# Performance work log

Measured on AMD Instinct MI355X. Metric: run time of the kernel, lower is better.

## Reference

```python
import jax, jax.numpy as jnp
import numpy as np


def setup_inputs() -> dict:
    key = jax.random.key(0)
    k1, k2 = jax.random.split(key)
    N, D = 8192, 256
    cond_feature = jax.random.normal(k1, (N, D), dtype=jnp.float32)
    sol_feature = jax.random.normal(k2, (N, D), dtype=jnp.float32)
    temperature = jnp.asarray(0.5, dtype=jnp.float32)  # learned scalar, used as exp(temperature)
    return {"cond_feature": cond_feature, "sol_feature": sol_feature, "temperature": temperature}


def reference(cond_feature, sol_feature, temperature):
    N = cond_feature.shape[0]
    c = cond_feature.reshape(N, -1)  # [N, D]
    s = sol_feature.reshape(sol_feature.shape[0], -1)  # [N, D]
    # pairwise L2 distance via ||a||^2 + ||b||^2 - 2 a.b (avoids N x N x D intermediate)
    c2 = jnp.sum(c * c, axis=-1)  # [N]
    s2 = jnp.sum(s * s, axis=-1)  # [N]
    d2 = c2[:, None] + s2[None, :] - 2.0 * jnp.einsum('nd,md->nm', c, s)
    dist = jnp.sqrt(jnp.maximum(d2, 0.0))  # [N, N]
    sim = -dist * jnp.exp(temperature)
    # cross_entropy(sim, arange) + cross_entropy(sim.T, arange): diagonal of log-softmax both ways
    logp_row = jax.nn.log_softmax(sim, axis=-1)  # CE over rows
    logp_col = jax.nn.log_softmax(sim, axis=0)   # CE over columns == CE(sim.T, labels)
    diag = jnp.arange(N)
    loss_row = -jnp.mean(logp_row[diag, diag])
    loss_col = -jnp.mean(logp_col[diag, diag])
    return (loss_row + loss_col) * 0.5
```

## Files before the change

kernel.cpp:

```cpp
#include <hip/hip_runtime.h>
#include <math.h>

#define DIM 256
#define TM 256
#define TN 128

typedef int   v4i   __attribute__((ext_vector_type(4)));
typedef int   v8i   __attribute__((ext_vector_type(8)));
typedef float f32x16 __attribute__((ext_vector_type(16)));

typedef const __attribute__((address_space(1))) void* gas_ptr;
typedef __attribute__((address_space(3))) void* las_ptr;

__device__ __forceinline__ void async_cp16(const void* g, void* l) {
    __builtin_amdgcn_global_load_lds((gas_ptr)g, (las_ptr)l, 16, 0, 0);
}

__global__ __launch_bounds__(256) void convert_kernel(
        const float* __restrict__ C, const float* __restrict__ S,
        unsigned char* __restrict__ Cb, unsigned char* __restrict__ Sb,
        float* __restrict__ c2, float* __restrict__ s2,
        float* __restrict__ ddot, float* __restrict__ sums0,
        float* __restrict__ out, int N) {
    int gtid = blockIdx.x * 256 + threadIdx.x;
    if (gtid < 2 * N) sums0[gtid] = 0.0f;
    if (gtid == 0) out[0] = 0.0f;
    int row = gtid >> 6;
    int l = gtid & 63;
    if (row >= N) return;
    float4 v  = ((const float4*)(C + (size_t)row * DIM))[l];
    float4 sv = ((const float4*)(S + (size_t)row * DIM))[l];
    int pc = __builtin_amdgcn_cvt_pk_fp8_f32(v.x, v.y, 0, false);
    pc     = __builtin_amdgcn_cvt_pk_fp8_f32(v.z, v.w, pc, true);
    int ps = __builtin_amdgcn_cvt_pk_fp8_f32(sv.x, sv.y, 0, false);
    ps     = __builtin_amdgcn_cvt_pk_fp8_f32(sv.z, sv.w, ps, true);
    int idx4 = (row >> 5) * 2048 + (l >> 4) * 512 + ((l >> 2) & 1) * 256
             + ((row & 31) + 32 * ((l >> 3) & 1)) * 4 + (l & 3);
    ((int*)Cb)[idx4] = pc;
    ((int*)Sb)[idx4] = ps;
    float nc = v.x * v.x + v.y * v.y + v.z * v.z + v.w * v.w;
    float ns = sv.x * sv.x + sv.y * sv.y + sv.z * sv.z + sv.w * sv.w;
    float cr = v.x * sv.x + v.y * sv.y + v.z * sv.z + v.w * sv.w;
    #pragma unroll
    for (int off = 32; off > 0; off >>= 1) {
        nc += __shfl_down(nc, off, 64);
        ns += __shfl_down(ns, off, 64);
        cr += __shfl_down(cr, off, 64);
    }
    if (l == 0) { c2[row] = nc; s2[row] = ns; ddot[row] = cr; }
}

__global__ __launch_bounds__(512, 4) void mfma_kernel(
        const unsigned char* __restrict__ Cb, const unsigned char* __restrict__ Sb,
        const float* __restrict__ c2, const float* __restrict__ s2,
        const float* __restrict__ temp,
        float* __restrict__ rowsum, float* __restrict__ colsum, int N) {
    __shared__ __align__(16) unsigned char Abuf[TM * 64];
    __shared__ __align__(16) unsigned char Bbuf[TN * 64];
    __shared__ float rs[TM], cs[TN], c2t[TM], s2t[TN];

    const int tid = threadIdx.x;
    const int bm = blockIdx.y * TM;
    const int bn = blockIdx.x * TN;
    const int w  = tid >> 6;
    const int l  = tid & 63;
    const int wm = (w >> 1) * 64;
    const int wn = (w & 1) * 64;

    const float escale = __expf(temp[0]);
    const float Kf = escale * 1.4426950408889634f;
    const float K2 = Kf * Kf;
    const float m2K2 = -2.0f * K2;

    if (tid < TM) { rs[tid] = 0.0f; c2t[tid] = K2 * c2[bm + tid]; }
    else if (tid < TM + TN) {
        int t = tid - TM; cs[t] = 0.0f; s2t[t] = K2 * s2[bn + t];
    }

    const unsigned char* gA = Cb + (size_t)((bm >> 5) + w) * 8192 + (size_t)l * 16;
    const unsigned char* gB = Sb + (size_t)((bn >> 5) + (w >> 1)) * 8192
                                 + (size_t)(w & 1) * 1024 + (size_t)l * 16;
    unsigned char* lA = &Abuf[w * 2048];
    unsigned char* lB = &Bbuf[(w >> 1) * 2048 + (w & 1) * 1024];

    const int abase = (w >> 1) * 4096 + l * 16;
    const int bbase = (w & 1) * 4096 + l * 16;

    f32x16 acc[2][2] = {};

    #pragma unroll
    for (int kk = 0; kk < 4; ++kk) {
        async_cp16(gA, lA);
        async_cp16(gA + 1024, lA + 1024);
        async_cp16(gB, lB);
        gA += 2048; gB += 2048;
        __syncthreads();

        v8i af[2], bf[2];
        #pragma unroll
        for (int t = 0; t < 2; ++t) {
            v4i alo = *(const v4i*)&Abuf[abase + t * 2048];
            v4i ahi = *(const v4i*)&Abuf[abase + t * 2048 + 1024];
            af[t] = __builtin_shufflevector(alo, ahi, 0, 1, 2, 3, 4, 5, 6, 7);
            v4i blo = *(const v4i*)&Bbuf[bbase + t * 2048];
            v4i bhi = *(const v4i*)&Bbuf[bbase + t * 2048 + 1024];
            bf[t] = __builtin_shufflevector(blo, bhi, 0, 1, 2, 3, 4, 5, 6, 7);
        }
        #pragma unroll
        for (int mi = 0; mi < 2; ++mi)
            #pragma unroll
            for (int ni = 0; ni < 2; ++ni)
                acc[mi][ni] = __builtin_amdgcn_mfma_scale_f32_32x32x64_f8f6f4(
                    af[mi], bf[ni], acc[mi][ni], 0, 0,
                    0, 0x7F, 0, 0x7F);
        __syncthreads();
    }

    const int q2 = l >> 5;
    const int col5 = l & 31;
    float s2v[2] = { s2t[wn + col5], s2t[wn + 32 + col5] };

    float rfold[2];
    float cp[2] = {0.f, 0.f};

    #pragma unroll
    for (int mi = 0; mi < 2; ++mi) {
        float c2r[16];
        #pragma unroll
        for (int s = 0; s < 16; ++s)
            c2r[s] = c2t[wm + mi * 32 + (s & 3) + 8 * (s >> 2) + 4 * q2];
        float rp[16];
        #pragma unroll
        for (int s = 0; s < 16; ++s) rp[s] = 0.0f;
        #pragma unroll
        for (int ni = 0; ni < 2; ++ni) {
            #pragma unroll
            for (int s = 0; s < 16; ++s) {
                float d2 = fmaf(m2K2, acc[mi][ni][s], c2r[s] + s2v[ni]);
                d2 = fmaxf(d2, 0.0f);
                float e = __builtin_amdgcn_exp2f(-__builtin_amdgcn_sqrtf(d2));
                rp[s] += e;
                cp[ni] += e;
            }
        }
        #pragma unroll
        for (int b = 0; b < 4; ++b) {
            const int n = 16 >> b;
            const int bit = (l >> b) & 1;
            #pragma unroll
            for (int k = 0; k < 8; ++k) {
                if (k < (n >> 1)) {
                    float keep = bit ? rp[2 * k + 1] : rp[2 * k];
                    float send = bit ? rp[2 * k] : rp[2 * k + 1];
                    rp[k] = keep + __shfl_xor(send, 1 << b, 64);
                }
            }
        }
        rfold[mi] = rp[0];
    }
    const int mymi = (l >> 4) & 1;
    {
        float keep = mymi ? rfold[1] : rfold[0];
        float send = mymi ? rfold[0] : rfold[1];
        float rfin = keep + __shfl_xor(send, 16, 64);
        const int s = l & 15;
        const int myrow = wm + mymi * 32 + (s & 3) + 8 * (s >> 2) + 4 * q2;
        atomicAdd(&rs[myrow], rfin);
    }
    {
        float keep = q2 ? cp[1] : cp[0];
        float send = q2 ? cp[0] : cp[1];
        float cfin = keep + __shfl_xor(send, 32, 64);
        atomicAdd(&cs[wn + q2 * 32 + col5], cfin);
    }

    __syncthreads();
    if (tid < TM) atomicAdd(&rowsum[bm + tid], rs[tid]);
    else if (tid < TM + TN) atomicAdd(&colsum[bn + tid - TM], cs[tid - TM]);
}

__global__ __launch_bounds__(256) void finalize_kernel(
        const float* __restrict__ rowsum, const float* __restrict__ colsum,
        const float* __restrict__ c2, const float* __restrict__ s2,
        const float* __restrict__ ddot, const float* __restrict__ temp,
        float* __restrict__ out, int N) {
    __shared__ float red[4];
    const float escale = __expf(temp[0]);
    const int tid = threadIdx.x;
    int i = blockIdx.x * 256 + tid;
    float sum = 0.0f;
    if (i < N) {
        float d2 = c2[i] + s2[i] - 2.0f * ddot[i];
        float dist = __builtin_amdgcn_sqrtf(fmaxf(d2, 0.0f));
        sum = __logf(rowsum[i]) + __logf(colsum[i]) + 2.0f * escale * dist;
    }
    #pragma unroll
    for (int off = 32; off > 0; off >>= 1) sum += __shfl_down(sum, off, 64);
    if ((tid & 63) == 0) red[tid >> 6] = sum;
    __syncthreads();
    if (tid == 0)
        atomicAdd(out, (red[0] + red[1] + red[2] + red[3]) / (2.0f * (float)N));
}

extern "C" void kernel_launch(void* const* d_in, const int* in_sizes, int n_in,
                              void* d_out, int out_size, void* d_ws, size_t ws_size,
                              hipStream_t stream) {
    const float* C = (const float*)d_in[0];
    const float* S = (const float*)d_in[1];
    const float* T = (const float*)d_in[2];
    const int N = in_sizes[0] / DIM;

    float* ws     = (float*)d_ws;
    float* c2     = ws;
    float* s2     = ws + N;
    float* rowsum = ws + 2 * N;
    float* colsum = ws + 3 * N;
    float* ddot   = ws + 4 * N;
    unsigned char* Cb = (unsigned char*)(ws + 5 * N + 64);
    unsigned char* Sb = Cb + (size_t)N * DIM;

    convert_kernel<<<(N * 64) / 256, 256, 0, stream>>>(
        C, S, Cb, Sb, c2, s2, ddot, rowsum, (float*)d_out, N);

    dim3 grid(N / TN, N / TM);
    mfma_kernel<<<grid, 512, 0, stream>>>(
        Cb, Sb, c2, s2, T, rowsum, colsum, N);

    finalize_kernel<<<(N + 255) / 256, 256, 0, stream>>>(
        rowsum, colsum, c2, s2, ddot, T, (float*)d_out, N);
}
```

Before: 113.4 us.

## Load FP8 MFMA fragments directly from global memory, dropping LDS staging

The MFMA kernel no longer stages A/B tiles through LDS with global_load_lds and per-k-step barriers. Each wave now reads its fragments straight from the pre-swizzled global FP8 layout. The tile shrinks to 128x128 with 256 threads, and the launch bounds change to (256, 3). This removes the LDS traffic and barrier stalls, but operands shared between waves are now fetched redundantly from L2/global, and there are twice as many blocks, each doing its own atomics.

```diff
diff --git a/kernel.cpp b/kernel.cpp
--- a/kernel.cpp
+++ b/kernel.cpp
@@ -2,19 +2,12 @@
 #include <math.h>
 
 #define DIM 256
-#define TM 256
+#define TM 128
 #define TN 128
 
-typedef int   v4i   __attribute__((ext_vector_type(4)));
-typedef int   v8i   __attribute__((ext_vector_type(8)));
+typedef int   v4i    __attribute__((ext_vector_type(4)));
+typedef int   v8i    __attribute__((ext_vector_type(8)));
 typedef float f32x16 __attribute__((ext_vector_type(16)));
-
-typedef const __attribute__((address_space(1))) void* gas_ptr;
-typedef __attribute__((address_space(3))) void* las_ptr;
-
-__device__ __forceinline__ void async_cp16(const void* g, void* l) {
-    __builtin_amdgcn_global_load_lds((gas_ptr)g, (las_ptr)l, 16, 0, 0);
-}
 
 __global__ __launch_bounds__(256) void convert_kernel(
         const float* __restrict__ C, const float* __restrict__ S,
@@ -50,13 +43,11 @@
     if (l == 0) { c2[row] = nc; s2[row] = ns; ddot[row] = cr; }
 }
 
-__global__ __launch_bounds__(512, 4) void mfma_kernel(
+__global__ __launch_bounds__(256, 3) void mfma_kernel(
         const unsigned char* __restrict__ Cb, const unsigned char* __restrict__ Sb,
         const float* __restrict__ c2, const float* __restrict__ s2,
         const float* __restrict__ temp,
         float* __restrict__ rowsum, float* __restrict__ colsum, int N) {
-    __shared__ __align__(16) unsigned char Abuf[TM * 64];
-    __shared__ __align__(16) unsigned char Bbuf[TN * 64];
     __shared__ float rs[TM], cs[TN], c2t[TM], s2t[TN];
 
     const int tid = threadIdx.x;
@@ -73,37 +64,24 @@
     const float m2K2 = -2.0f * K2;
 
     if (tid < TM) { rs[tid] = 0.0f; c2t[tid] = K2 * c2[bm + tid]; }
-    else if (tid < TM + TN) {
-        int t = tid - TM; cs[t] = 0.0f; s2t[t] = K2 * s2[bn + t];
-    }
-
-    const unsigned char* gA = Cb + (size_t)((bm >> 5) + w) * 8192 + (size_t)l * 16;
-    const unsigned char* gB = Sb + (size_t)((bn >> 5) + (w >> 1)) * 8192
-                                 + (size_t)(w & 1) * 1024 + (size_t)l * 16;
-    unsigned char* lA = &Abuf[w * 2048];
-    unsigned char* lB = &Bbuf[(w >> 1) * 2048 + (w & 1) * 1024];
-
-    const int abase = (w >> 1) * 4096 + l * 16;
-    const int bbase = (w & 1) * 4096 + l * 16;
+    else { int t = tid - TM; cs[t] = 0.0f; s2t[t] = K2 * s2[bn + t]; }
+    __syncthreads();
+
+    const unsigned char* baseA = Cb + (size_t)((bm + wm) >> 5) * 8192 + l * 16;
+    const unsigned char* baseB = Sb + (size_t)((bn + wn) >> 5) * 8192 + l * 16;
 
     f32x16 acc[2][2] = {};
 
     #pragma unroll
     for (int kk = 0; kk < 4; ++kk) {
-        async_cp16(gA, lA);
-        async_cp16(gA + 1024, lA + 1024);
-        async_cp16(gB, lB);
-        gA += 2048; gB += 2048;
-        __syncthreads();
-
         v8i af[2], bf[2];
         #pragma unroll
         for (int t = 0; t < 2; ++t) {
-            v4i alo = *(const v4i*)&Abuf[abase + t * 2048];
-            v4i ahi = *(const v4i*)&Abuf[abase + t * 2048 + 1024];
+            v4i alo = *(const v4i*)(baseA + t * 8192 + kk * 2048);
+            v4i ahi = *(const v4i*)(baseA + t * 8192 + kk * 2048 + 1024);
             af[t] = __builtin_shufflevector(alo, ahi, 0, 1, 2, 3, 4, 5, 6, 7);
-            v4i blo = *(const v4i*)&Bbuf[bbase + t * 2048];
-            v4i bhi = *(const v4i*)&Bbuf[bbase + t * 2048 + 1024];
+            v4i blo = *(const v4i*)(baseB + t * 8192 + kk * 2048);
+            v4i bhi = *(const v4i*)(baseB + t * 8192 + kk * 2048 + 1024);
             bf[t] = __builtin_shufflevector(blo, bhi, 0, 1, 2, 3, 4, 5, 6, 7);
         }
         #pragma unroll
@@ -113,7 +91,6 @@
                 acc[mi][ni] = __builtin_amdgcn_mfma_scale_f32_32x32x64_f8f6f4(
                     af[mi], bf[ni], acc[mi][ni], 0, 0,
                     0, 0x7F, 0, 0x7F);
-        __syncthreads();
     }
 
     const int q2 = l >> 5;
@@ -176,7 +153,7 @@
 
     __syncthreads();
     if (tid < TM) atomicAdd(&rowsum[bm + tid], rs[tid]);
-    else if (tid < TM + TN) atomicAdd(&colsum[bn + tid - TM], cs[tid - TM]);
+    else atomicAdd(&colsum[bn + tid - TM], cs[tid - TM]);
 }
 
 __global__ __launch_bounds__(256) void finalize_kernel(
@@ -223,7 +200,7 @@
         C, S, Cb, Sb, c2, s2, ddot, rowsum, (float*)d_out, N);
 
     dim3 grid(N / TN, N / TM);
-    mfma_kernel<<<grid, 512, 0, stream>>>(
+    mfma_kernel<<<grid, 256, 0, stream>>>(
         Cb, Sb, c2, s2, T, rowsum, colsum, N);
 
     finalize_kernel<<<(N + 255) / 256, 256, 0, stream>>>(
```

Result: faster. 105.6 us (-6.8%).
